# Optimization experiments

Hardware: AMD Instinct MI355X
Metric: run time of the kernel (lower is better)

The kernel has to match this reference:

```python
import jax, jax.numpy as jnp
import numpy as np

PZ = 16          # partition_size
SMOOTH = 1e-8


def setup_inputs() -> dict:
    key = jax.random.key(0)
    k1, k2, k3, k4 = jax.random.split(key, 4)
    shape = (4, 2, 160, 160, 160)  # [N, C, Z, X, Y]
    pred = jax.random.uniform(k1, shape, dtype=jnp.float32)
    groundtruth = jax.random.uniform(k2, shape, dtype=jnp.float32)
    a = jax.random.uniform(k3, (1,), dtype=jnp.float32)
    b = jax.random.uniform(k4, (1,), dtype=jnp.float32)
    return {"pred": pred, "groundtruth": groundtruth, "a": a, "b": b}


def _blocks(t):
    # [N,C,Z,X,Y] -> rows of per-(block, channel) voxels [N*nz*nx*ny*C, PZ^3]
    # matches the torch loops: blocks ordered (N, zz, xx, yy) with channel dim
    # of each block concatenated along dim 0 before flattening dims 1..-1.
    N, C, Z, X, Y = t.shape
    nz, nx, ny = Z // PZ, X // PZ, Y // PZ
    t = t.reshape(N, C, nz, PZ, nx, PZ, ny, PZ)
    t = t.transpose(0, 2, 4, 6, 1, 3, 5, 7)  # [N,nz,nx,ny,C,pz,pz,pz]
    return t.reshape(N * nz * nx * ny * C, PZ * PZ * PZ)


def reference(pred, groundtruth, a, b):
    p = _blocks(pred)
    g = _blocks(groundtruth)
    tp = jnp.sum(g * p, axis=1)
    fn = jnp.sum(g * (1.0 - p), axis=1)
    fp = jnp.sum((1.0 - g) * p, axis=1)
    denom = fp + fn + SMOOTH
    alpha = a + b * ((fp + SMOOTH) / denom)
    beta = a + b * ((fn + SMOOTH) / denom)
    loss = jnp.sum(1.0 - (tp + SMOOTH) / (tp + alpha * fp + beta * fn + SMOOTH))
    return loss
```

## Files before the change

kernel.cpp:

```cpp
#include <hip/hip_runtime.h>

#define PZ 16
#define SMOOTH 1e-8f

constexpr int Nn = 4, Cc = 2, Zz = 160, Xx = 160, Yy = 160;
constexpr int NZ = Zz / PZ, NX = Xx / PZ, NY = Yy / PZ;
constexpr int NBLK = Nn * NZ * NX * NY * Cc;

__global__ void zero_out_kernel(float* out) { out[0] = 0.0f; }

__global__ __launch_bounds__(256)
void adaloss_kernel(const float* __restrict__ pred,
                    const float* __restrict__ gt,
                    const float* __restrict__ a_p,
                    const float* __restrict__ b_p,
                    float* __restrict__ out)
{
    int bid = blockIdx.x;
    int c   = bid % Cc;  int t1 = bid / Cc;
    int yyb = t1 % NY;   t1 /= NY;
    int xxb = t1 % NX;   t1 /= NX;
    int zzb = t1 % NZ;   int n = t1 / NZ;

    const long base =
        ((((long)(n * Cc + c) * Zz + zzb * PZ) * Xx + xxb * PZ) * Yy + yyb * PZ);

    const int t    = threadIdx.x;
    const int zofs = t >> 6;
    const int idx  = t & 63;
    const int xl   = idx >> 2;
    const int v    = idx & 3;

    float sp = 0.0f, sg = 0.0f, sgp = 0.0f;

    #pragma unroll
    for (int pass = 0; pass < 4; ++pass) {
        const int  zp  = zofs + pass * 4;
        const long off = base + (long)zp * (Xx * Yy) + (long)xl * Yy + v * 4;
        const float4 p = *reinterpret_cast<const float4*>(pred + off);
        const float4 g = *reinterpret_cast<const float4*>(gt + off);
        sp  += p.x + p.y + p.z + p.w;
        sg  += g.x + g.y + g.z + g.w;
        sgp += p.x * g.x + p.y * g.y + p.z * g.z + p.w * g.w;
    }

    #pragma unroll
    for (int s = 32; s > 0; s >>= 1) {
        sp  += __shfl_down(sp,  s, 64);
        sg  += __shfl_down(sg,  s, 64);
        sgp += __shfl_down(sgp, s, 64);
    }

    __shared__ float red[3][4];
    const int wave = t >> 6;
    const int lane = t & 63;
    if (lane == 0) { red[0][wave] = sp; red[1][wave] = sg; red[2][wave] = sgp; }
    __syncthreads();

    if (t == 0) {
        const float SP  = red[0][0] + red[0][1] + red[0][2] + red[0][3];
        const float SG  = red[1][0] + red[1][1] + red[1][2] + red[1][3];
        const float SGP = red[2][0] + red[2][1] + red[2][2] + red[2][3];

        const float tp = SGP;
        const float fn = SG - SGP;
        const float fp = SP - SGP;

        const float a = a_p[0];
        const float b = b_p[0];

        const float denom = fp + fn + SMOOTH;
        const float alpha = a + b * ((fp + SMOOTH) / denom);
        const float beta  = a + b * ((fn + SMOOTH) / denom);
        const float term  =
            1.0f - (tp + SMOOTH) / (tp + alpha * fp + beta * fn + SMOOTH);

        atomicAdd(out, term);
    }
}

extern "C" void kernel_launch(void* const* d_in, const int* in_sizes, int n_in,
                              void* d_out, int out_size, void* d_ws, size_t ws_size,
                              hipStream_t stream)
{
    const float* pred = (const float*)d_in[0];
    const float* gt   = (const float*)d_in[1];
    const float* a_p  = (const float*)d_in[2];
    const float* b_p  = (const float*)d_in[3];
    float* out = (float*)d_out;

    zero_out_kernel<<<1, 1, 0, stream>>>(out);
    adaloss_kernel<<<NBLK, 256, 0, stream>>>(pred, gt, a_p, b_p, out);
}
```

Baseline: 307.5 us.

## Restructure into full-row contiguous loads with LDS staging and workspace partial sums

Each workgroup now handles a 4-plane z-slab of one 16-row x-strip across the whole y extent (640 float4 per plane). It loads fully contiguous rows, double-buffers them through shared memory, and reduces per-yy-block partials into a workspace with atomics. A separate finalize kernel computes the loss terms and sums them. This replaces the old layout, where each workgroup read scattered 64-byte segments, and is meant to improve coalescing and DRAM streaming. The cost is two extra launches, extra atomics and shared-memory synchronisation.

After: 298.5 us. 1.03x faster.

```diff
diff --git a/kernel.cpp b/kernel.cpp
--- a/kernel.cpp
+++ b/kernel.cpp
@@ -1,82 +1,133 @@
 #include <hip/hip_runtime.h>
 
-#define PZ 16
 #define SMOOTH 1e-8f
 
 constexpr int Nn = 4, Cc = 2, Zz = 160, Xx = 160, Yy = 160;
-constexpr int NZ = Zz / PZ, NX = Xx / PZ, NY = Yy / PZ;
-constexpr int NBLK = Nn * NZ * NX * NY * Cc;
+constexpr int NB = 10;
+constexpr int NROWS = Nn * NB * NB * NB * Cc;
+constexpr int WG1 = Nn * Cc * NB * NB * 4;
 
-__global__ void zero_out_kernel(float* out) { out[0] = 0.0f; }
+__global__ void zero_ws_kernel(float* ws, float* out) {
+    int i = blockIdx.x * 256 + threadIdx.x;
+    if (i < NROWS * 3) ws[i] = 0.f;
+    if (i == 0) out[0] = 0.f;
+}
+
+__global__ __launch_bounds__(256, 6)
+void partial_kernel(const float* __restrict__ pred,
+                    const float* __restrict__ gt,
+                    float* __restrict__ ws)
+{
+    __shared__ float4 sp_[640];
+    __shared__ float4 sg_[640];
+
+    int wg = blockIdx.x;
+    const int c  = wg & 1;  wg >>= 1;
+    const int q4 = wg & 3;  wg >>= 2;
+    const int xx = wg % 10; wg /= 10;
+    const int zz = wg % 10;
+    const int n  = wg / 10;
+
+    const int t = threadIdx.x;
+    const int zbase = zz * 16 + q4 * 4;
+
+    const long planeStride = 6400L;
+    const long base0 = ((long)((n * 2 + c) * 160 + zbase) * 160 + xx * 16) * 40L;
+
+    const float4* p4 = reinterpret_cast<const float4*>(pred);
+    const float4* g4 = reinterpret_cast<const float4*>(gt);
+
+    float4 rp0, rp1, rp2, rg0, rg1, rg2;
+    const bool third = (t < 128);
+
+    auto LOADS = [&](int s) {
+        const float4* pb = p4 + base0 + (long)s * planeStride;
+        const float4* gb = g4 + base0 + (long)s * planeStride;
+        rp0 = pb[t]; rp1 = pb[t + 256]; if (third) rp2 = pb[t + 512];
+        rg0 = gb[t]; rg1 = gb[t + 256]; if (third) rg2 = gb[t + 512];
+    };
+    auto WRITE = [&]() {
+        sp_[t] = rp0; sp_[t + 256] = rp1; if (third) sp_[t + 512] = rp2;
+        sg_[t] = rg0; sg_[t + 256] = rg1; if (third) sg_[t + 512] = rg2;
+    };
+
+    const int l = t >> 4, v = t & 15;
+
+    float asp0 = 0, asg0 = 0, agp0 = 0;
+    float asp1 = 0, asg1 = 0, agp1 = 0;
+    float asp2 = 0, asg2 = 0, agp2 = 0;
+
+    auto dotacc = [&](int idx, float& SP, float& SG, float& GP) {
+        float4 p = sp_[idx], g = sg_[idx];
+        SP += (p.x + p.y) + (p.z + p.w);
+        SG += (g.x + g.y) + (g.z + g.w);
+        GP += p.x * g.x + p.y * g.y + p.z * g.z + p.w * g.w;
+    };
+
+    LOADS(0);
+    for (int s = 0; s < 4; ++s) {
+        __syncthreads();
+        WRITE();
+        if (s < 3) LOADS(s + 1);
+        __syncthreads();
+        const int i0 = l * 40 + v;
+        dotacc(i0,      asp0, asg0, agp0);
+        dotacc(i0 + 16, asp1, asg1, agp1);
+        if (v < 8) dotacc(i0 + 32, asp2, asg2, agp2);
+    }
+    __syncthreads();
+
+#define RED4(x) x += __shfl_xor(x, 1, 64); x += __shfl_xor(x, 2, 64); \
+                x += __shfl_xor(x, 16, 64); x += __shfl_xor(x, 32, 64);
+    RED4(asp0) RED4(asg0) RED4(agp0)
+    RED4(asp1) RED4(asg1) RED4(agp1)
+    RED4(asp2) RED4(asg2) RED4(agp2)
+#undef RED4
+
+    float* red = reinterpret_cast<float*>(sp_);
+    const int lane = t & 63, wave = t >> 6;
+    if ((lane & 51) == 0) {
+        const int q = lane >> 2;
+        float* dst = red + (wave * 4 + q) * 9;
+        dst[0] = asp0; dst[1] = asg0; dst[2] = agp0;
+        dst[3] = asp1; dst[4] = asg1; dst[5] = agp1;
+        dst[6] = asp2; dst[7] = asg2; dst[8] = agp2;
+    }
+    __syncthreads();
+
+    if (t < 30) {
+        const int yy = t / 3, sidx = t % 3;
+        const int q = yy & 3, j = yy >> 2;
+        float val = 0.f;
+        #pragma unroll
+        for (int w = 0; w < 4; ++w) val += red[(w * 4 + q) * 9 + j * 3 + sidx];
+        const int row = (((n * 10 + zz) * 10 + xx) * 10 + yy) * 2 + c;
+        atomicAdd(&ws[row * 3 + sidx], val);
+    }
+}
 
 __global__ __launch_bounds__(256)
-void adaloss_kernel(const float* __restrict__ pred,
-                    const float* __restrict__ gt,
-                    const float* __restrict__ a_p,
-                    const float* __restrict__ b_p,
-                    float* __restrict__ out)
+void finalize_kernel(const float* __restrict__ ws,
+                     const float* __restrict__ a_p,
+                     const float* __restrict__ b_p,
+                     float* __restrict__ out)
 {
-    int bid = blockIdx.x;
-    int c   = bid % Cc;  int t1 = bid / Cc;
-    int yyb = t1 % NY;   t1 /= NY;
-    int xxb = t1 % NX;   t1 /= NX;
-    int zzb = t1 % NZ;   int n = t1 / NZ;
-
-    const long base =
-        ((((long)(n * Cc + c) * Zz + zzb * PZ) * Xx + xxb * PZ) * Yy + yyb * PZ);
-
-    const int t    = threadIdx.x;
-    const int zofs = t >> 6;
-    const int idx  = t & 63;
-    const int xl   = idx >> 2;
-    const int v    = idx & 3;
-
-    float sp = 0.0f, sg = 0.0f, sgp = 0.0f;
-
-    #pragma unroll
-    for (int pass = 0; pass < 4; ++pass) {
-        const int  zp  = zofs + pass * 4;
-        const long off = base + (long)zp * (Xx * Yy) + (long)xl * Yy + v * 4;
-        const float4 p = *reinterpret_cast<const float4*>(pred + off);
-        const float4 g = *reinterpret_cast<const float4*>(gt + off);
-        sp  += p.x + p.y + p.z + p.w;
-        sg  += g.x + g.y + g.z + g.w;
-        sgp += p.x * g.x + p.y * g.y + p.z * g.z + p.w * g.w;
-    }
-
-    #pragma unroll
-    for (int s = 32; s > 0; s >>= 1) {
-        sp  += __shfl_down(sp,  s, 64);
-        sg  += __shfl_down(sg,  s, 64);
-        sgp += __shfl_down(sgp, s, 64);
-    }
-
-    __shared__ float red[3][4];
-    const int wave = t >> 6;
-    const int lane = t & 63;
-    if (lane == 0) { red[0][wave] = sp; red[1][wave] = sg; red[2][wave] = sgp; }
-    __syncthreads();
-
-    if (t == 0) {
-        const float SP  = red[0][0] + red[0][1] + red[0][2] + red[0][3];
-        const float SG  = red[1][0] + red[1][1] + red[1][2] + red[1][3];
-        const float SGP = red[2][0] + red[2][1] + red[2][2] + red[2][3];
-
+    const int r = blockIdx.x * 256 + threadIdx.x;
+    float term = 0.f;
+    if (r < NROWS) {
+        const float SP = ws[r * 3], SG = ws[r * 3 + 1], SGP = ws[r * 3 + 2];
         const float tp = SGP;
         const float fn = SG - SGP;
         const float fp = SP - SGP;
-
-        const float a = a_p[0];
-        const float b = b_p[0];
-
+        const float a = a_p[0], b = b_p[0];
         const float denom = fp + fn + SMOOTH;
         const float alpha = a + b * ((fp + SMOOTH) / denom);
         const float beta  = a + b * ((fn + SMOOTH) / denom);
-        const float term  =
-            1.0f - (tp + SMOOTH) / (tp + alpha * fp + beta * fn + SMOOTH);
-
-        atomicAdd(out, term);
+        term = 1.f - (tp + SMOOTH) / (tp + alpha * fp + beta * fn + SMOOTH);
     }
+    #pragma unroll
+    for (int d = 32; d > 0; d >>= 1) term += __shfl_down(term, d, 64);
+    if ((threadIdx.x & 63) == 0) atomicAdd(out, term);
 }
 
 extern "C" void kernel_launch(void* const* d_in, const int* in_sizes, int n_in,
@@ -88,7 +139,9 @@
     const float* a_p  = (const float*)d_in[2];
     const float* b_p  = (const float*)d_in[3];
     float* out = (float*)d_out;
+    float* ws  = (float*)d_ws;
 
-    zero_out_kernel<<<1, 1, 0, stream>>>(out);
-    adaloss_kernel<<<NBLK, 256, 0, stream>>>(pred, gt, a_p, b_p, out);
+    zero_ws_kernel<<<(NROWS * 3 + 255) / 256, 256, 0, stream>>>(ws, out);
+    partial_kernel<<<WG1, 256, 0, stream>>>(pred, gt, ws);
+    finalize_kernel<<<32, 256, 0, stream>>>(ws, a_p, b_p, out);
 }
```

## Read full contiguous Y rows per workgroup and finalize loss in separate kernel

Applied to the files above, without the earlier changes.

The single per-block kernel reading 64-byte row fragments is replaced by a partial-sum kernel where each workgroup streams four full z-slices of a 16-row x-slab, each row spanning the whole Y extent, as contiguous float4 loads. It stages per-float4 sums in shared memory, reduces them per y-block with wave shuffles, and writes partial sums to workspace. A second kernel combines the four z-quarters per block, computes the loss term, and does one atomic per wave instead of one per block. The intent is to turn the strided short-segment reads into long coalesced reads for better DRAM efficiency. The cost is an extra launch, a workspace round trip, and shared-memory pressure from about 30 KB per workgroup.

Result: faster. 283.5 us (-7.8%).

```diff
diff --git a/kernel.cpp b/kernel.cpp
--- a/kernel.cpp
+++ b/kernel.cpp
@@ -1,82 +1,115 @@
 #include <hip/hip_runtime.h>
 
-#define PZ 16
 #define SMOOTH 1e-8f
 
-constexpr int Nn = 4, Cc = 2, Zz = 160, Xx = 160, Yy = 160;
-constexpr int NZ = Zz / PZ, NX = Xx / PZ, NY = Yy / PZ;
-constexpr int NBLK = Nn * NZ * NX * NY * Cc;
+constexpr int NROWS = 8000;
+constexpr int WG1   = 3200;
 
 __global__ void zero_out_kernel(float* out) { out[0] = 0.0f; }
 
-__global__ __launch_bounds__(256)
-void adaloss_kernel(const float* __restrict__ pred,
+__global__ __launch_bounds__(256, 5)
+void partial_kernel(const float* __restrict__ pred,
                     const float* __restrict__ gt,
-                    const float* __restrict__ a_p,
-                    const float* __restrict__ b_p,
-                    float* __restrict__ out)
+                    float* __restrict__ wsq)
 {
-    int bid = blockIdx.x;
-    int c   = bid % Cc;  int t1 = bid / Cc;
-    int yyb = t1 % NY;   t1 /= NY;
-    int xxb = t1 % NX;   t1 /= NX;
-    int zzb = t1 % NZ;   int n = t1 / NZ;
+    __shared__ float spA[2560], sgA[2560], gpA[2560];
+    __shared__ float red[4][30];
 
-    const long base =
-        ((((long)(n * Cc + c) * Zz + zzb * PZ) * Xx + xxb * PZ) * Yy + yyb * PZ);
+    int wg = blockIdx.x;
+    const int q4 = wg & 3;  wg >>= 2;
+    const int c  = wg & 1;  wg >>= 1;
+    const int xx = wg % 10; wg /= 10;
+    const int zz = wg % 10;
+    const int n  = wg / 10;
 
-    const int t    = threadIdx.x;
-    const int zofs = t >> 6;
-    const int idx  = t & 63;
-    const int xl   = idx >> 2;
-    const int v    = idx & 3;
+    const int t = threadIdx.x;
+    const long base0 = ((long)((n * 2 + c) * 160 + zz * 16 + q4 * 4) * 160 + xx * 16) * 40L;
 
-    float sp = 0.0f, sg = 0.0f, sgp = 0.0f;
+    const float4* p4 = reinterpret_cast<const float4*>(pred);
+    const float4* g4 = reinterpret_cast<const float4*>(gt);
 
     #pragma unroll
-    for (int pass = 0; pass < 4; ++pass) {
-        const int  zp  = zofs + pass * 4;
-        const long off = base + (long)zp * (Xx * Yy) + (long)xl * Yy + v * 4;
-        const float4 p = *reinterpret_cast<const float4*>(pred + off);
-        const float4 g = *reinterpret_cast<const float4*>(gt + off);
-        sp  += p.x + p.y + p.z + p.w;
-        sg  += g.x + g.y + g.z + g.w;
-        sgp += p.x * g.x + p.y * g.y + p.z * g.z + p.w * g.w;
+    for (int s = 0; s < 10; ++s) {
+        const int  v   = s * 256 + t;
+        const int  zp  = v / 640;
+        const int  rem = v - zp * 640;
+        const long a   = base0 + (long)zp * 6400 + rem;
+        const float4 p = p4[a];
+        const float4 g = g4[a];
+        spA[v] = (p.x + p.y) + (p.z + p.w);
+        sgA[v] = (g.x + g.y) + (g.z + g.w);
+        gpA[v] = p.x * g.x + p.y * g.y + p.z * g.z + p.w * g.w;
+    }
+    __syncthreads();
+
+    const int cell  = t >> 2;
+    const int q     = t & 3;
+    const int sbase = (cell >> 4) * 640 + (cell & 15) * 40 + q;
+
+    float aS[10], aG[10], aP[10];
+    #pragma unroll
+    for (int yy = 0; yy < 10; ++yy) {
+        const int s = sbase + yy * 4;
+        aS[yy] = spA[s]; aG[yy] = sgA[s]; aP[yy] = gpA[s];
+    }
+    #pragma unroll
+    for (int yy = 0; yy < 10; ++yy) {
+        #pragma unroll
+        for (int d = 1; d < 64; d <<= 1) {
+            aS[yy] += __shfl_xor(aS[yy], d, 64);
+            aG[yy] += __shfl_xor(aG[yy], d, 64);
+            aP[yy] += __shfl_xor(aP[yy], d, 64);
+        }
     }
 
-    #pragma unroll
-    for (int s = 32; s > 0; s >>= 1) {
-        sp  += __shfl_down(sp,  s, 64);
-        sg  += __shfl_down(sg,  s, 64);
-        sgp += __shfl_down(sgp, s, 64);
+    const int lane = t & 63, wave = t >> 6;
+    if (lane == 0) {
+        #pragma unroll
+        for (int yy = 0; yy < 10; ++yy) {
+            red[wave][yy * 3 + 0] = aS[yy];
+            red[wave][yy * 3 + 1] = aG[yy];
+            red[wave][yy * 3 + 2] = aP[yy];
+        }
     }
-
-    __shared__ float red[3][4];
-    const int wave = t >> 6;
-    const int lane = t & 63;
-    if (lane == 0) { red[0][wave] = sp; red[1][wave] = sg; red[2][wave] = sgp; }
     __syncthreads();
 
-    if (t == 0) {
-        const float SP  = red[0][0] + red[0][1] + red[0][2] + red[0][3];
-        const float SG  = red[1][0] + red[1][1] + red[1][2] + red[1][3];
-        const float SGP = red[2][0] + red[2][1] + red[2][2] + red[2][3];
+    if (t < 30) {
+        const float val = red[0][t] + red[1][t] + red[2][t] + red[3][t];
+        const int yy   = t / 3;
+        const int comp = t - yy * 3;
+        const int row  = (((n * 10 + zz) * 10 + xx) * 10 + yy) * 2 + c;
+        wsq[(row * 4 + q4) * 3 + comp] = val;
+    }
+}
+
+__global__ __launch_bounds__(256)
+void finalize_kernel(const float* __restrict__ wsq,
+                     const float* __restrict__ a_p,
+                     const float* __restrict__ b_p,
+                     float* __restrict__ out)
+{
+    const int r = blockIdx.x * 256 + threadIdx.x;
+    float term = 0.f;
+    if (r < NROWS) {
+        const float4 w0 = *reinterpret_cast<const float4*>(wsq + r * 12);
+        const float4 w1 = *reinterpret_cast<const float4*>(wsq + r * 12 + 4);
+        const float4 w2 = *reinterpret_cast<const float4*>(wsq + r * 12 + 8);
+        const float SP  = w0.x + w0.w + w1.z + w2.y;
+        const float SG  = w0.y + w1.x + w1.w + w2.z;
+        const float SGP = w0.z + w1.y + w2.x + w2.w;
 
         const float tp = SGP;
         const float fn = SG - SGP;
         const float fp = SP - SGP;
-
-        const float a = a_p[0];
-        const float b = b_p[0];
-
+        const float a = a_p[0], b = b_p[0];
         const float denom = fp + fn + SMOOTH;
         const float alpha = a + b * ((fp + SMOOTH) / denom);
         const float beta  = a + b * ((fn + SMOOTH) / denom);
-        const float term  =
-            1.0f - (tp + SMOOTH) / (tp + alpha * fp + beta * fn + SMOOTH);
-
-        atomicAdd(out, term);
+        term = 1.f - (tp + SMOOTH) / (tp + alpha * fp + beta * fn + SMOOTH);
     }
+    #pragma unroll
+    for (int d = 32; d > 0; d >>= 1) term += __shfl_down(term, d, 64);
+    if ((threadIdx.x & 63) == 0) atomicAdd(out, term);
 }
 
 extern "C" void kernel_launch(void* const* d_in, const int* in_sizes, int n_in,
@@ -88,7 +121,9 @@
     const float* a_p  = (const float*)d_in[2];
     const float* b_p  = (const float*)d_in[3];
     float* out = (float*)d_out;
+    float* wsq = (float*)d_ws;
 
     zero_out_kernel<<<1, 1, 0, stream>>>(out);
-    adaloss_kernel<<<NBLK, 256, 0, stream>>>(pred, gt, a_p, b_p, out);
+    partial_kernel<<<WG1, 256, 0, stream>>>(pred, gt, wsq);
+    finalize_kernel<<<(NROWS + 255) / 256, 256, 0, stream>>>(wsq, a_p, b_p, out);
 }
```
